# Optimization experiments

Measured on AMD Instinct MI355X. Metric: run time of the kernel, lower is better.

Reference implementation:

```python
import jax, jax.numpy as jnp
import numpy as np

ENC_L, DEC_L = 4, 6
H = 8
D = 512
DFF = 2048
DLAT = 128
NTOK = 1024
NCODES = 2048
NGROUPS = 64
DG = DLAT // NGROUPS  # 2
T_ENC, BT, NSEQ = 128, 8, 16
T_DEC = 1024


def sinusoid_pe(T, d):
    pos = jnp.arange(T, dtype=jnp.float32)[:, None]
    div = jnp.exp(jnp.arange(0, d, 2, dtype=jnp.float32) * (-jnp.log(10000.0) / d))
    pe = jnp.zeros((T, d), jnp.float32)
    pe = pe.at[:, 0::2].set(jnp.sin(pos * div))
    pe = pe.at[:, 1::2].set(jnp.cos(pos * div))
    return pe[:, None, :]  # [T,1,d], seq-first broadcast over batch


def layer_norm(x, g, b):
    m = x.mean(-1, keepdims=True)
    v = ((x - m) ** 2).mean(-1, keepdims=True)
    return (x - m) * jax.lax.rsqrt(v + 1e-5) * g + b


def mha(x, Wqkv, Wo, causal):
    T, B, d = x.shape
    dh = d // H
    q, k, v = jnp.split(x @ Wqkv, 3, axis=-1)
    q = q.reshape(T, B, H, dh)
    k = k.reshape(T, B, H, dh)
    v = v.reshape(T, B, H, dh)
    scores = jnp.einsum('tbhd,sbhd->bhts', q, k) / jnp.sqrt(jnp.float32(dh))
    if causal:
        mask = jnp.tril(jnp.ones((T, T), bool))
        scores = jnp.where(mask[None, None], scores, jnp.float32(-1e9))
    attn = jax.nn.softmax(scores, axis=-1)
    out = jnp.einsum('bhts,sbhd->tbhd', attn, v).reshape(T, B, d)
    return out @ Wo


def tf_layer(x, p, i, causal):
    Wqkv, Wo, ln1g, ln1b, ln2g, ln2b, W1, b1, W2, b2 = [a[i] for a in p]
    x = layer_norm(x + mha(x, Wqkv, Wo, causal), ln1g, ln1b)
    h = jax.nn.relu(x @ W1 + b1) @ W2 + b2
    return layer_norm(x + h, ln2g, ln2b)


def forward_core(enc_inp, dec_inp, dec_inp_seq_pos, fl):
    (emb_table,
     eWqkv, eWo, eln1g, eln1b, eln2g, eln2b, eW1, eb1, eW2, eb2,
     dWqkv, dWo, dln1g, dln1b, dln2g, dln2b, dW1, db1, dW2, db2,
     W_mu, b_mu, codebook, seg_W, seg_b, W_out, b_out) = fl
    scale = jnp.sqrt(jnp.float32(D))
    # token embeddings (seq-first)
    enc_emb = emb_table[enc_inp] * scale            # [T_ENC, BT, NSEQ, D]
    dec_emb = emb_table[dec_inp] * scale            # [T_DEC, BT, D]
    x = enc_emb.reshape(T_ENC, BT * NSEQ, D) + sinusoid_pe(T_ENC, D)
    y = dec_emb + sinusoid_pe(T_DEC, D)
    enc_p = (eWqkv, eWo, eln1g, eln1b, eln2g, eln2b, eW1, eb1, eW2, eb2)
    for i in range(ENC_L):
        x = tf_layer(x, enc_p, i, False)
    mu = x[0] @ W_mu + b_mu                         # [BT*NSEQ, DLAT]
    # grouped vector quantization
    g = mu.reshape(-1, NGROUPS, DG)
    d2 = (g ** 2).sum(-1, keepdims=True) - 2.0 * jnp.einsum('bgd,cd->bgc', g, codebook) + (codebook ** 2).sum(-1)
    idx = jnp.argmin(d2, axis=-1)                   # [BT*NSEQ, NGROUPS]
    q = codebook[idx]
    sg = jax.lax.stop_gradient
    diff = jnp.mean((sg(q) - g) ** 2) + jnp.mean((q - sg(g)) ** 2)
    z = (g + sg(q - g)).reshape(-1, DLAT)           # straight-through
    # ragged scatter of per-segment latents into decoder timeline (vectorized)
    lat = z.reshape(BT, NSEQ, DLAT)
    t = jnp.arange(T_DEC)
    seg = jax.vmap(lambda p: jnp.searchsorted(p, t, side='right') - 1)(dec_inp_seq_pos)  # [BT, T_DEC]
    valid = (seg >= 0) & (seg < NSEQ)
    segc = jnp.clip(seg, 0, NSEQ - 1)
    dec_seg = jnp.where(valid[..., None], lat[jnp.arange(BT)[:, None], segc], 0.0)  # [BT, T_DEC, DLAT]
    dec_seg_emb = dec_seg.transpose(1, 0, 2)        # [T_DEC, BT, DLAT]
    # decoder with in-attention segment conditioning at every layer
    seg_proj = dec_seg_emb @ seg_W + seg_b          # [T_DEC, BT, D]
    dec_p = (dWqkv, dWo, dln1g, dln1b, dln2g, dln2b, dW1, db1, dW2, db2)
    for i in range(DEC_L):
        y = tf_layer(y + seg_proj, dec_p, i, True)
    logits = y @ W_out + b_out                      # [T_DEC, BT, NTOK]
    return mu, z, diff, logits


def setup_inputs() -> dict:
    key = jax.random.key(0)
    ks = jax.random.split(key, 16)
    rn = lambda k, shape, s=0.02: jax.random.normal(k, shape, jnp.float32) * s
    inp = {}
    inp['enc_inp'] = jax.random.randint(ks[0], (T_ENC, BT, NSEQ), 0, NTOK)
    inp['dec_inp'] = jax.random.randint(ks[1], (T_DEC, BT), 0, NTOK)
    inp['dec_inp_seq_pos'] = jnp.sort(jax.random.randint(ks[2], (BT, NSEQ + 1), 0, T_DEC), axis=-1)
    inp['emb_table'] = rn(ks[3], (NTOK, D))
    def stack(kk, L):
        sk = jax.random.split(kk, 4)
        return dict(Wqkv=rn(sk[0], (L, D, 3 * D)), Wo=rn(sk[1], (L, D, D)),
                    ln1g=jnp.ones((L, D)), ln1b=jnp.zeros((L, D)),
                    ln2g=jnp.ones((L, D)), ln2b=jnp.zeros((L, D)),
                    W1=rn(sk[2], (L, D, DFF)), b1=jnp.zeros((L, DFF)),
                    W2=rn(sk[3], (L, DFF, D)), b2=jnp.zeros((L, D)))
    for nm, v in stack(ks[4], ENC_L).items():
        inp['enc_' + nm] = v
    for nm, v in stack(ks[5], DEC_L).items():
        inp['dec_' + nm] = v
    inp['W_mu'] = rn(ks[6], (D, DLAT)); inp['b_mu'] = jnp.zeros((DLAT,))
    inp['codebook'] = rn(ks[7], (NCODES, DG), 1.0)
    inp['seg_W'] = rn(ks[8], (DLAT, D)); inp['seg_b'] = jnp.zeros((D,))
    inp['W_out'] = rn(ks[9], (D, NTOK)); inp['b_out'] = jnp.zeros((NTOK,))
    return inp


def reference(enc_inp, dec_inp, dec_inp_seq_pos, emb_table,
              enc_Wqkv, enc_Wo, enc_ln1g, enc_ln1b, enc_ln2g, enc_ln2b, enc_W1, enc_b1, enc_W2, enc_b2,
              dec_Wqkv, dec_Wo, dec_ln1g, dec_ln1b, dec_ln2g, dec_ln2b, dec_W1, dec_b1, dec_W2, dec_b2,
              W_mu, b_mu, codebook, seg_W, seg_b, W_out, b_out):
    fl = (emb_table,
          enc_Wqkv, enc_Wo, enc_ln1g, enc_ln1b, enc_ln2g, enc_ln2b, enc_W1, enc_b1, enc_W2, enc_b2,
          dec_Wqkv, dec_Wo, dec_ln1g, dec_ln1b, dec_ln2g, dec_ln2b, dec_W1, dec_b1, dec_W2, dec_b2,
          W_mu, b_mu, codebook, seg_W, seg_b, W_out, b_out)
    return forward_core(enc_inp, dec_inp, dec_inp_seq_pos, fl)
```

## Files before the change

### kernel.cpp

```cpp
#include <hip/hip_runtime.h>
#include <hip/hip_bf16.h>


using bf16 = __hip_bfloat16;

#define ENC_L 4
#define DEC_L 6
#define NH    8
#define DMODEL 512
#define DH    64
#define DFF   2048
#define DLAT  128
#define NTOK  1024
#define NCODES 2048
#define T_ENC 128
#define BT    8
#define NSEQ  16
#define T_DEC 1024
#define BENC  (BT*NSEQ)
#define EMB_SCALE 22.627416997969522f
#define LN10000 9.210340371976184f

#define MC 2048
#define ENC_CB 16
// ... 311 lines not shown
        lmax = fmaxf(lmax, dsum);
    }
    red[tid] = lmax; __syncthreads();
    for (int o = 128; o > 0; o >>= 1) {
        if (tid < o) red[tid] = fmaxf(red[tid], red[tid + o]);
        __syncthreads();
    }
    float m = red[0]; __syncthreads();
    float lsum = 0.f;
    for (int s = tid; s < Tlim; s += 256) {
        float e = expf(sc[s] - m);
        sc[s] = e;
        lsum += e;
    }
    red[tid] = lsum; __syncthreads();
    for (int o = 128; o > 0; o >>= 1) {
        if (tid < o) red[tid] += red[tid + o];
        __syncthreads();
    }
    float inv = 1.f / red[0];
    int d = tid & 63, grp = tid >> 6;
    float a = 0.f;
    for (int s = grp; s < Tlim; s += 4)
        a += sc[s] * qkv[((size_t)bl * T + s) * (3 * DMODEL) + 2 * DMODEL + h * DH + d];
    part[tid] = a; __syncthreads();
    if (tid < 64) {
        float o = (part[tid] + part[tid + 64] + part[tid + 128] + part[tid + 192]) * inv;
        out[row * DMODEL + h * DH + tid] = o;
    }
}

__global__ __launch_bounds__(256) void ln_res_kernel(
    const float* __restrict__ a, const float* __restrict__ c,
    const void* __restrict__ g, const void* __restrict__ be, size_t goff,
    float* __restrict__ out, const int* __restrict__ dflag)
{
    int isbf = dflag[0];
    __shared__ float red[256];
    int row = blockIdx.x, tid = threadIdx.x;
    size_t base = (size_t)row * DMODEL;
    float x0 = a[base + tid] + c[base + tid];
    float x1 = a[base + tid + 256] + c[base + tid + 256];
    red[tid] = x0 + x1; __syncthreads();
    for (int o = 128; o > 0; o >>= 1) {
        if (tid < o) red[tid] += red[tid + o];
        __syncthreads();
    }
    float mean = red[0] * (1.f / DMODEL); __syncthreads();
    float d0 = x0 - mean, d1 = x1 - mean;
    red[tid] = d0 * d0 + d1 * d1; __syncthreads();
    for (int o = 128; o > 0; o >>= 1) {
        if (tid < o) red[tid] += red[tid + o];
        __syncthreads();
    }
    float rstd = rsqrtf(red[0] * (1.f / DMODEL) + 1e-5f);
    out[base + tid] = d0 * rstd * ldw(g, goff + tid, isbf) + ldw(be, goff + tid, isbf);
    out[base + tid + 256] = d1 * rstd * ldw(g, goff + tid + 256, isbf) + ldw(be, goff + tid + 256, isbf);
}

__global__ __launch_bounds__(128) void seg_kernel(
    const int* __restrict__ pos, const float* __restrict__ z,
    float* __restrict__ dsc, int b0)
{
    int t = blockIdx.x, bl = blockIdx.y;
    int b = b0 + bl;
    __shared__ int sseg;
    if (threadIdx.x == 0) {
        int cnt = 0;
        for (int i = 0; i < NSEQ + 1; i++) cnt += (pos[b * (NSEQ + 1) + i] <= t) ? 1 : 0;
        sseg = cnt - 1;
    }
    __syncthreads();
    int seg = sseg;
    float v = 0.f;
    if (seg >= 0 && seg < NSEQ) v = z[(b * NSEQ + seg) * DLAT + threadIdx.x];
    dsc[((size_t)bl * T_DEC + t) * DLAT + threadIdx.x] = v;
}


__global__ __launch_bounds__(256) void conv_w_kernel(
    const void* __restrict__ W, unsigned short* __restrict__ WhT,
    unsigned short* __restrict__ WlT, int K, int N, const int* __restrict__ dflag)
{
    int isbf = dflag[0];
    __shared__ float tile[32][33];
    size_t base = (size_t)blockIdx.z * K * N;
    int k0 = blockIdx.y * 32, n0 = blockIdx.x * 32;
    int tx = threadIdx.x & 31, ty = threadIdx.x >> 5;
    #pragma unroll
    for (int i = 0; i < 4; i++)
        tile[ty + 8 * i][tx] = ldw(W, base + (size_t)(k0 + ty + 8 * i) * N + n0 + tx, isbf);
    __syncthreads();
    #pragma unroll
    for (int i = 0; i < 4; i++) {
        float v = tile[tx][ty + 8 * i];
        unsigned short h = f2bf_rne(v);
        size_t o = base + (size_t)(n0 + ty + 8 * i) * K + k0 + tx;
        WhT[o] = h;
        WlT[o] = f2bf_rne(v - bf2f(h));
    }
}

__global__ void conv_vec_kernel(const void* __restrict__ src, float* __restrict__ dst,
                                int n, const int* __restrict__ dflag) {
    int i = blockIdx.x * 256 + threadIdx.x;
    if (i < n) dst[i] = ldw(src, i, dflag[0]);
}

__global__ void embed2_kernel(const int* __restrict__ toks, const void* __restrict__ emb,
                              float* __restrict__ out, unsigned short* __restrict__ oh,
                              unsigned short* __restrict__ ol,
                              int T, int Bdim, int bj0, int total,
                              const int* __restrict__ dflag) {
    int isbf = dflag[0];
    int idx = blockIdx.x * 256 + threadIdx.x;
    if (idx >= total) return;
    int row = idx >> 9;
    int d = idx & 511;
    int bl = row / T;
    int t = row - bl * T;
    int tok = toks[t * Bdim + bj0 + bl];
    float v = ldw(emb, (size_t)tok * DMODEL + d, isbf) * EMB_SCALE;
    int j = d >> 1;
    float freq = expf(-(float)(2 * j) * (LN10000 / (float)DMODEL));
    float ang = (float)t * freq;
    v += (d & 1) ? cosf(ang) : sinf(ang);
    out[idx] = v;
    unsigned short h = f2bf_rne(v);
    oh[idx] = h;
    ol[idx] = f2bf_rne(v - bf2f(h));
}

__global__ void add2_kernel(const float* __restrict__ a, const float* __restrict__ b,
                            float* __restrict__ c, unsigned short* __restrict__ ch,
                            unsigned short* __restrict__ cl, int n) {
    int i = blockIdx.x * 256 + threadIdx.x;
    if (i >= n) return;
    float v = a[i] + b[i];
    c[i] = v;
    unsigned short h = f2bf_rne(v);
    ch[i] = h;
    cl[i] = f2bf_rne(v - bf2f(h));
}

__global__ void gather2_kernel(const float* __restrict__ Xc,
                               unsigned short* __restrict__ agh,
                               unsigned short* __restrict__ agl, int bj0) {
    int bl = blockIdx.x;
    int d = threadIdx.x;
    #pragma unroll
    for (int k = 0; k < 2; k++) {
        int dd = d + k * 256;
        float v = Xc[(size_t)bl * T_ENC * DMODEL + dd];
        size_t o = (size_t)(bj0 + bl) * DMODEL + dd;
        unsigned short h = f2bf_rne(v);
        agh[o] = h;
        agl[o] = f2bf_rne(v - bf2f(h));
    }
}

__global__ __launch_bounds__(128) void seg2_kernel(
    const int* __restrict__ pos, const float* __restrict__ z,
    unsigned short* __restrict__ dh, unsigned short* __restrict__ dl, int b0)
{
    int t = blockIdx.x, bl = blockIdx.y;
    int b = b0 + bl;
    __shared__ int sseg;
    if (threadIdx.x == 0) {
        int cnt = 0;
        for (int i = 0; i < NSEQ + 1; i++) cnt += (pos[b * (NSEQ + 1) + i] <= t) ? 1 : 0;
        sseg = cnt - 1;
    }
    __syncthreads();
    int seg = sseg;
    float v = 0.f;
    if (seg >= 0 && seg < NSEQ) v = z[(b * NSEQ + seg) * DLAT + threadIdx.x];
    size_t o = ((size_t)bl * T_DEC + t) * DLAT + threadIdx.x;
    unsigned short h = f2bf_rne(v);
    dh[o] = h;
    dl[o] = f2bf_rne(v - bf2f(h));
}

__global__ __launch_bounds__(256) void ln_res2_kernel(
    const float* __restrict__ a, const float* __restrict__ c,
    const float* __restrict__ g, const float* __restrict__ be, size_t goff,
    float* __restrict__ out, unsigned short* __restrict__ oh,
    unsigned short* __restrict__ ol)
{
    __shared__ float red[256];
    int row = blockIdx.x, tid = threadIdx.x;
    size_t base = (size_t)row * DMODEL;
    float x0 = a[base + tid] + c[base + tid];
    float x1 = a[base + tid + 256] + c[base + tid + 256];
    red[tid] = x0 + x1; __syncthreads();
    for (int o = 128; o > 0; o >>= 1) {
        if (tid < o) red[tid] += red[tid + o];
        __syncthreads();
    }
    float mean = red[0] * (1.f / DMODEL); __syncthreads();
    float d0 = x0 - mean, d1 = x1 - mean;
    red[tid] = d0 * d0 + d1 * d1; __syncthreads();
    for (int o = 128; o > 0; o >>= 1) {
        if (tid < o) red[tid] += red[tid + o];
        __syncthreads();
    }
    float rstd = rsqrtf(red[0] * (1.f / DMODEL) + 1e-5f);
    float o0 = d0 * rstd * g[goff + tid] + be[goff + tid];
    float o1 = d1 * rstd * g[goff + tid + 256] + be[goff + tid + 256];
    out[base + tid] = o0;
    out[base + tid + 256] = o1;
    unsigned short h0 = f2bf_rne(o0);
    oh[base + tid] = h0;
    ol[base + tid] = f2bf_rne(o0 - bf2f(h0));
    unsigned short h1 = f2bf_rne(o1);
    oh[base + tid + 256] = h1;
    ol[base + tid + 256] = f2bf_rne(o1 - bf2f(h1));
}

__global__ __launch_bounds__(256) void gemm_hl_kernel(
    const unsigned short* __restrict__ Ah, const unsigned short* __restrict__ Al,
    const unsigned short* __restrict__ Wh, const unsigned short* __restrict__ Wl,
    size_t woff, const float* __restrict__ bias, size_t boff,
    float* __restrict__ C, unsigned short* __restrict__ Ch, unsigned short* __restrict__ Cl,
    int M, int N, int K, int relu, int wmode, int b0perm,
    const int* __restrict__ dflag)
{
    int isbf = dflag[0];
    __shared__ unsigned short sAh[4096], sAl[4096], sBh[4096], sBl[4096];
    int tid = threadIdx.x;
    int lane = tid & 63, wave = tid >> 6, quad = lane >> 4, l15 = lane & 15;
    int wm = (wave >> 1) * 32, wn = (wave & 1) * 32;
    int row0 = blockIdx.y * 64, col0 = blockIdx.x * 64;
    int sr = tid >> 3, sc = (tid & 7) * 8;

    floatx4 acc[2][2];
    #pragma unroll
    for (int i = 0; i < 2; i++)
        #pragma unroll
        for (int j = 0; j < 2; j++)
            acc[i][j] = (floatx4){0.f, 0.f, 0.f, 0.f};

    const unsigned short* Wbh = Wh + woff;
    const unsigned short* Wbl = Wl + woff;

    for (int k0 = 0; k0 < K; k0 += 64) {
        #pragma unroll
        for (int rnd = 0; rnd < 2; rnd++) {
            int r = rnd * 32 + sr;
            size_t ga = (size_t)(row0 + r) * K + k0 + sc;
            size_t gb = (size_t)(col0 + r) * K + k0 + sc;
            int di = SWZ(r, sc);
            *(short8*)&sAh[di] = *(const short8*)(const void*)(Ah + ga);
            *(short8*)&sAl[di] = *(const short8*)(const void*)(Al + ga);
            *(short8*)&sBh[di] = *(const short8*)(const void*)(Wbh + gb);
            if (!isbf)
                *(short8*)&sBl[di] = *(const short8*)(const void*)(Wbl + gb);
        }
        __syncthreads();
        if (isbf) {
            #pragma unroll
            for (int ks = 0; ks < 64; ks += 32) {
                short8 fah[2], fal[2], fbh[2];
                #pragma unroll
                for (int i = 0; i < 2; i++) {
                    fah[i] = *(const short8*)&sAh[SWZ(wm + i * 16 + l15, ks + quad * 8)];
                    fal[i] = *(const short8*)&sAl[SWZ(wm + i * 16 + l15, ks + quad * 8)];
                    fbh[i] = *(const short8*)&sBh[SWZ(wn + i * 16 + l15, ks + quad * 8)];
                }
                #pragma unroll
                for (int i = 0; i < 2; i++)
                    #pragma unroll
                    for (int j = 0; j < 2; j++) {
                        acc[i][j] = __builtin_amdgcn_mfma_f32_16x16x32_bf16(fah[i], fbh[j], acc[i][j], 0, 0, 0);
                        acc[i][j] = __builtin_amdgcn_mfma_f32_16x16x32_bf16(fal[i], fbh[j], acc[i][j], 0, 0, 0);
                    }
            }
        } else {
            #pragma unroll
            for (int ks = 0; ks < 64; ks += 32) {
                short8 fah[2], fal[2], fbh[2], fbl[2];
                #pragma unroll
                for (int i = 0; i < 2; i++) {
                    fah[i] = *(const short8*)&sAh[SWZ(wm + i * 16 + l15, ks + quad * 8)];
                    fal[i] = *(const short8*)&sAl[SWZ(wm + i * 16 + l15, ks + quad * 8)];
                    fbh[i] = *(const short8*)&sBh[SWZ(wn + i * 16 + l15, ks + quad * 8)];
                    fbl[i] = *(const short8*)&sBl[SWZ(wn + i * 16 + l15, ks + quad * 8)];
                }
                #pragma unroll
                for (int i = 0; i < 2; i++)
                    #pragma unroll
                    for (int j = 0; j < 2; j++) {
                        acc[i][j] = __builtin_amdgcn_mfma_f32_16x16x32_bf16(fah[i], fbh[j], acc[i][j], 0, 0, 0);
                        acc[i][j] = __builtin_amdgcn_mfma_f32_16x16x32_bf16(fal[i], fbh[j], acc[i][j], 0, 0, 0);
                        acc[i][j] = __builtin_amdgcn_mfma_f32_16x16x32_bf16(fah[i], fbl[j], acc[i][j], 0, 0, 0);
                    }
            }
        }
        __syncthreads();
    }
    #pragma unroll
    for (int i = 0; i < 2; i++) {
        #pragma unroll
        for (int j = 0; j < 2; j++) {
            int gc = col0 + wn + j * 16 + l15;
            float bv = bias ? bias[boff + gc] : 0.f;
            #pragma unroll
            for (int r = 0; r < 4; r++) {
                int gr = row0 + wm + i * 16 + quad * 4 + r;
                float v = acc[i][j][r] + bv;
                if (relu) v = fmaxf(v, 0.f);
                size_t orow = (size_t)gr;
                if (b0perm >= 0) orow = (size_t)((gr & (T_DEC - 1)) * BT + b0perm + (gr >> 10));
                if (wmode & 1) C[orow * N + gc] = v;
                if (wmode & 2) {
                    unsigned short hh = f2bf_rne(v);
                    Ch[(size_t)gr * N + gc] = hh;
                    Cl[(size_t)gr * N + gc] = f2bf_rne(v - bf2f(hh));
                }
            }
        }
    }
}

__global__ __launch_bounds__(256) void v_prep_kernel(
    const unsigned short* __restrict__ QKVh, const unsigned short* __restrict__ QKVl,
    unsigned short* __restrict__ VhT, unsigned short* __restrict__ VlT, int T)
{
    __shared__ unsigned short th[64][72], tl[64][72];
    int tid = threadIdx.x;
    int r0 = blockIdx.x * 64;
    int vc0 = blockIdx.y * 64;
    int sr = tid >> 3, sc = (tid & 7) * 8;
    #pragma unroll
    for (int rnd = 0; rnd < 2; rnd++) {
        int rr = rnd * 32 + sr;
        size_t o = (size_t)(r0 + rr) * 1536 + 1024 + vc0 + sc;
        *(short8*)&th[rr][sc] = *(const short8*)(const void*)(QKVh + o);
        *(short8*)&tl[rr][sc] = *(const short8*)(const void*)(QKVl + o);
    }
    __syncthreads();
    int bl = r0 / T;
    int t0 = r0 - bl * T;
    #pragma unroll
    for (int rnd = 0; rnd < 2; rnd++) {
        int dr = rnd * 32 + sr;
        int gd = vc0 + dr;
        int hh = gd >> 6, dd = gd & 63;
        size_t obase = ((size_t)(bl * NH + hh) * 64 + dd) * T + t0 + sc;
        short8 hv, lv;
        #pragma unroll
        for (int i = 0; i < 8; i++) {
            hv[i] = (short)th[sc + i][dr];
            lv[i] = (short)tl[sc + i][dr];
        }
        *(short8*)&VhT[obase] = hv;
        *(short8*)&VlT[obase] = lv;
    }
}

__global__ __launch_bounds__(256) void attn_flash_kernel(
    const unsigned short* __restrict__ QKVh, const unsigned short* __restrict__ QKVl,
    const unsigned short* __restrict__ VhT, const unsigned short* __restrict__ VlT,
    unsigned short* __restrict__ AOh, unsigned short* __restrict__ AOl,
    int T, int causal)
{
    __shared__ unsigned short sQh[4096], sQl[4096], sKh[4096], sKl[4096],
                              sVh[4096], sVl[4096], sPh[4096], sPl[4096];
    int tid = threadIdx.x;
    int lane = tid & 63, wave = tid >> 6, quad = lane >> 4, l15 = lane & 15;
    int q0 = blockIdx.x * 64;
    int bl = blockIdx.y >> 3, h = blockIdx.y & 7;
    int sr = tid >> 3, sc = (tid & 7) * 8;
    int wq = wave * 16;
    size_t rowbase = (size_t)bl * T;
    size_t vbase = (size_t)(bl * NH + h) * 64;

    #pragma unroll
    for (int rnd = 0; rnd < 2; rnd++) {
        int r = rnd * 32 + sr;
        size_t o = (rowbase + q0 + r) * 1536 + h * 64 + sc;
        int di = SWZ(r, sc);
        *(short8*)&sQh[di] = *(const short8*)(const void*)(QKVh + o);
        *(short8*)&sQl[di] = *(const short8*)(const void*)(QKVl + o);
    }

    floatx4 acco[4];
    #pragma unroll
    for (int jd = 0; jd < 4; jd++) acco[jd] = (floatx4){0.f, 0.f, 0.f, 0.f};
    float m_old[4], lsum[4];
    #pragma unroll
    for (int r = 0; r < 4; r++) { m_old[r] = -1e30f; lsum[r] = 0.f; }

    int smax = causal ? q0 : (T - 64);
    for (int s0 = 0; s0 <= smax; s0 += 64) {
        #pragma unroll
        for (int rnd = 0; rnd < 2; rnd++) {
            int r = rnd * 32 + sr;
            int di = SWZ(r, sc);
            size_t ko = (rowbase + s0 + r) * 1536 + 512 + h * 64 + sc;
            *(short8*)&sKh[di] = *(const short8*)(const void*)(QKVh + ko);
            *(short8*)&sKl[di] = *(const short8*)(const void*)(QKVl + ko);
            size_t vo = (vbase + r) * T + s0 + sc;
            *(short8*)&sVh[di] = *(const short8*)(const void*)(VhT + vo);
            *(short8*)&sVl[di] = *(const short8*)(const void*)(VlT + vo);
        }
        __syncthreads();

        floatx4 accs[4];
        #pragma unroll
        for (int j = 0; j < 4; j++) accs[j] = (floatx4){0.f, 0.f, 0.f, 0.f};
        #pragma unroll
        for (int ks = 0; ks < 64; ks += 32) {
            short8 qh = *(const short8*)&sQh[SWZ(wq + l15, ks + quad * 8)];
            short8 ql = *(const short8*)&sQl[SWZ(wq + l15, ks + quad * 8)];
            #pragma unroll
            for (int j = 0; j < 4; j++) {
                short8 kh = *(const short8*)&sKh[SWZ(j * 16 + l15, ks + quad * 8)];
                short8 kl = *(const short8*)&sKl[SWZ(j * 16 + l15, ks + quad * 8)];
                accs[j] = __builtin_amdgcn_mfma_f32_16x16x32_bf16(qh, kh, accs[j], 0, 0, 0);
                accs[j] = __builtin_amdgcn_mfma_f32_16x16x32_bf16(ql, kh, accs[j], 0, 0, 0);
                accs[j] = __builtin_amdgcn_mfma_f32_16x16x32_bf16(qh, kl, accs[j], 0, 0, 0);
            }
        }

        float f[4];
        #pragma unroll
        for (int r = 0; r < 4; r++) {
            int qg = q0 + wq + quad * 4 + r;
            float tm = -1e30f;
            #pragma unroll
            for (int j = 0; j < 4; j++) {
                float s = accs[j][r] * 0.125f;
                if (causal && (s0 + j * 16 + l15 > qg)) s = -1e30f;
                accs[j][r] = s;
                tm = fmaxf(tm, s);
            }
            #pragma unroll
            for (int mk = 1; mk < 16; mk <<= 1)
                tm = fmaxf(tm, __shfl_xor(tm, mk, 64));
            float mn = fmaxf(m_old[r], tm);
            float fr = __expf(m_old[r] - mn);
            float ts = 0.f;
            #pragma unroll
            for (int j = 0; j < 4; j++) {
                float p = __expf(accs[j][r] - mn);
                accs[j][r] = p;
                ts += p;
            }
            #pragma unroll
            for (int mk = 1; mk < 16; mk <<= 1)
                ts += __shfl_xor(ts, mk, 64);
            lsum[r] = lsum[r] * fr + ts;
            m_old[r] = mn;
            f[r] = fr;
        }
        #pragma unroll
        for (int jd = 0; jd < 4; jd++)
            #pragma unroll
            for (int r = 0; r < 4; r++)
                acco[jd][r] *= f[r];

        #pragma unroll
        for (int j = 0; j < 4; j++)
            #pragma unroll
            for (int r = 0; r < 4; r++) {
                float p = accs[j][r];
                unsigned short ph = f2bf_rne(p);
                int idx = SWZ(wq + quad * 4 + r, j * 16 + l15);
                sPh[idx] = ph;
                sPl[idx] = f2bf_rne(p - bf2f(ph));
            }
        __syncthreads();

        #pragma unroll
        for (int ks = 0; ks < 64; ks += 32) {
            short8 ph = *(const short8*)&sPh[SWZ(wq + l15, ks + quad * 8)];
            short8 pl = *(const short8*)&sPl[SWZ(wq + l15, ks + quad * 8)];
            #pragma unroll
            for (int jd = 0; jd < 4; jd++) {
                short8 vh = *(const short8*)&sVh[SWZ(jd * 16 + l15, ks + quad * 8)];
                short8 vl = *(const short8*)&sVl[SWZ(jd * 16 + l15, ks + quad * 8)];
                acco[jd] = __builtin_amdgcn_mfma_f32_16x16x32_bf16(ph, vh, acco[jd], 0, 0, 0);
                acco[jd] = __builtin_amdgcn_mfma_f32_16x16x32_bf16(pl, vh, acco[jd], 0, 0, 0);
                acco[jd] = __builtin_amdgcn_mfma_f32_16x16x32_bf16(ph, vl, acco[jd], 0, 0, 0);
            }
        }
        __syncthreads();
    }

    #pragma unroll
    for (int jd = 0; jd < 4; jd++) {
        #pragma unroll
        for (int r = 0; r < 4; r++) {
            int qr = q0 + wq + quad * 4 + r;
            float o = acco[jd][r] / lsum[r];
            size_t oo = (rowbase + qr) * 512 + h * 64 + jd * 16 + l15;
            unsigned short hh = f2bf_rne(o);
            AOh[oo] = hh;
            AOl[oo] = f2bf_rne(o - bf2f(hh));
        }
    }
}


static const size_t OFF_EWQKV = 0;
static const size_t OFF_EWO   = OFF_EWQKV + (size_t)4 * 512 * 1536;
static const size_t OFF_EW1   = OFF_EWO   + (size_t)4 * 512 * 512;
static const size_t OFF_EW2   = OFF_EW1   + (size_t)4 * 512 * 2048;
static const size_t OFF_DWQKV = OFF_EW2   + (size_t)4 * 2048 * 512;
static const size_t OFF_DWO   = OFF_DWQKV + (size_t)6 * 512 * 1536;
static const size_t OFF_DW1   = OFF_DWO   + (size_t)6 * 512 * 512;
static const size_t OFF_DW2   = OFF_DW1   + (size_t)6 * 512 * 2048;
static const size_t OFF_WMU   = OFF_DW2   + (size_t)6 * 2048 * 512;
static const size_t OFF_SEGW  = OFF_WMU   + (size_t)512 * 128;
static const size_t OFF_WOUT  = OFF_SEGW  + (size_t)128 * 512;
static const size_t W_TOTAL   = OFF_WOUT  + (size_t)512 * 1024;

static const size_t VELN1G = 0;
static const size_t VELN1B = VELN1G + 2048;
static const size_t VELN2G = VELN1B + 2048;
static const size_t VELN2B = VELN2G + 2048;
static const size_t VDLN1G = VELN2B + 2048;
static const size_t VDLN1B = VDLN1G + 3072;
static const size_t VDLN2G = VDLN1B + 3072;
static const size_t VDLN2B = VDLN2G + 3072;
static const size_t VEB1   = VDLN2B + 3072;
static const size_t VEB2   = VEB1 + 8192;
static const size_t VDB1   = VEB2 + 2048;
static const size_t VDB2   = VDB1 + 12288;
static const size_t VBMU   = VDB2 + 3072;
static const size_t VSEGB  = VBMU + 128;
static const size_t VBOUT  = VSEGB + 512;
static const size_t VEC_TOTAL = VBOUT + 1024;

extern "C" void kernel_launch(void* const* d_in, const int* in_sizes, int n_in,
                              void* d_out, int out_size, void* d_ws, size_t ws_size,
                              hipStream_t stream)
{
    const int*  enc_inp = (const int*)d_in[0];
    const int*  dec_inp = (const int*)d_in[1];
    const int*  seq_pos = (const int*)d_in[2];
    const void* emb   = d_in[3];
    const void* eWqkv = d_in[4];  const void* eWo  = d_in[5];
    const void* eln1g = d_in[6];  const void* eln1b = d_in[7];
    const void* eln2g = d_in[8];  const void* eln2b = d_in[9];
    const void* eW1   = d_in[10]; const void* eb1  = d_in[11];
    const void* eW2   = d_in[12]; const void* eb2  = d_in[13];
    const void* dWqkv = d_in[14]; const void* dWo  = d_in[15];
    const void* dln1g = d_in[16]; const void* dln1b = d_in[17];
    const void* dln2g = d_in[18]; const void* dln2b = d_in[19];
    const void* dW1   = d_in[20]; const void* db1  = d_in[21];
    const void* dW2   = d_in[22]; const void* db2  = d_in[23];
    const void* W_mu  = d_in[24]; const void* b_mu = d_in[25];
    const void* cbk   = d_in[26];
    const void* seg_W = d_in[27]; const void* seg_b = d_in[28];
    const void* W_out = d_in[29]; const void* b_out = d_in[30];

    float* outf = (float*)d_out;
    float* out_mu     = outf;
    float* out_z      = outf + 16384;
    float* out_diff   = outf + 32768;
    float* out_logits = outf + 32769;

    bool order_ok = (n_in == 31) &&
        in_sizes[0] == 16384 && in_sizes[1] == 8192 && in_sizes[2] == 136 &&
        in_sizes[3] == 524288 && in_sizes[4] == 3145728 && in_sizes[5] == 1048576 &&
        in_sizes[10] == 4194304 && in_sizes[14] == 4718592 && in_sizes[15] == 1572864 &&
        in_sizes[24] == 65536 && in_sizes[25] == 128 && in_sizes[26] == 4096 &&
        in_sizes[29] == 524288 && in_sizes[30] == 1024;
    if (!order_ok) {
        fill_kernel<<<64, 256, 0, stream>>>(out_mu, 100.0f, 16384);
        return;
    }

    float *XC = nullptr, *SPC = nullptr, *TIN = nullptr, *Pb = nullptr,
          *MU = nullptr, *Z = nullptr, *ACC = nullptr, *VECS = nullptr;
    unsigned short *XCh = nullptr, *XCl = nullptr, *TINh = nullptr, *TINl = nullptr,
                   *QKVh = nullptr, *QKVl = nullptr, *VhT = nullptr, *VlT = nullptr,
                   *AOh = nullptr, *AOl = nullptr, *Hh = nullptr, *Hl = nullptr,
                   *DSCh = nullptr, *DSCl = nullptr, *AGh = nullptr, *AGl = nullptr,
                   *WH = nullptr, *WL = nullptr;
    int* FLG = nullptr;

    auto layout = [&](size_t R) -> size_t {
        char* p = (char*)d_ws;
        auto al = [&](size_t b) -> char* {
            char* q = p; p += (b + 255) & ~(size_t)255; return q;
        };
        size_t Rd = R;
        XC   = (float*)al(R * 512 * 4);
        XCh  = (unsigned short*)al(R * 512 * 2);
        XCl  = (unsigned short*)al(R * 512 * 2);
        SPC  = (float*)al(Rd * 512 * 4);
        TIN  = (float*)al(Rd * 512 * 4);
        TINh = (unsigned short*)al(Rd * 512 * 2);
        TINl = (unsigned short*)al(Rd * 512 * 2);
        QKVh = (unsigned short*)al(R * 1536 * 2);
        QKVl = (unsigned short*)al(R * 1536 * 2);
        VhT  = (unsigned short*)al(R * 512 * 2);
        VlT  = (unsigned short*)al(R * 512 * 2);
        AOh  = (unsigned short*)al(R * 512 * 2);
        AOl  = (unsigned short*)al(R * 512 * 2);
        Pb   = (float*)al(R * 512 * 4);
        Hh   = (unsigned short*)al(R * 2048 * 2);
        Hl   = (unsigned short*)al(R * 2048 * 2);
        DSCh = (unsigned short*)al(Rd * 128 * 2);
        DSCl = (unsigned short*)al(Rd * 128 * 2);
        AGh  = (unsigned short*)al((size_t)128 * 512 * 2);
        AGl  = (unsigned short*)al((size_t)128 * 512 * 2);
        MU   = (float*)al((size_t)128 * 128 * 4);
        Z    = (float*)al((size_t)128 * 128 * 4);
        ACC  = (float*)al(256);
        FLG  = (int*)al(256);
        VECS = (float*)al(VEC_TOTAL * 4);
        WH   = (unsigned short*)al(W_TOTAL * 2);
        WL   = (unsigned short*)al(W_TOTAL * 2);
        return (size_t)(p - (char*)d_ws);
    };

    size_t R = 0;
    {
        const size_t cands[3] = {8192, 4096, 2048};
        for (int ci = 0; ci < 3; ci++) {
            if (layout(cands[ci]) <= ws_size) { R = cands[ci]; break; }
        }
    }

    if (R) {
        layout(R);
        int enc_cb = (int)(R / 128); if (enc_cb > 128) enc_cb = 128;
        int dec_cb = (int)(R / 1024); if (dec_cb > 8) dec_cb = 8;
        int rows_e = enc_cb * T_ENC;
        int rows_d = dec_cb * T_DEC;

        detect_kernel<<<1, 64, 0, stream>>>((const unsigned int*)eln1g, FLG, ACC);

        conv_w_kernel<<<dim3(1536/32, 512/32, 4), 256, 0, stream>>>(eWqkv, WH+OFF_EWQKV, WL+OFF_EWQKV, 512, 1536, FLG);
        conv_w_kernel<<<dim3( 512/32, 512/32, 4), 256, 0, stream>>>(eWo,   WH+OFF_EWO,   WL+OFF_EWO,   512,  512, FLG);
        conv_w_kernel<<<dim3(2048/32, 512/32, 4), 256, 0, stream>>>(eW1,   WH+OFF_EW1,   WL+OFF_EW1,   512, 2048, FLG);
        conv_w_kernel<<<dim3( 512/32,2048/32, 4), 256, 0, stream>>>(eW2,   WH+OFF_EW2,   WL+OFF_EW2,  2048,  512, FLG);
        conv_w_kernel<<<dim3(1536/32, 512/32, 6), 256, 0, stream>>>(dWqkv, WH+OFF_DWQKV, WL+OFF_DWQKV, 512, 1536, FLG);
        conv_w_kernel<<<dim3( 512/32, 512/32, 6), 256, 0, stream>>>(dWo,   WH+OFF_DWO,   WL+OFF_DWO,   512,  512, FLG);
        conv_w_kernel<<<dim3(2048/32, 512/32, 6), 256, 0, stream>>>(dW1,   WH+OFF_DW1,   WL+OFF_DW1,   512, 2048, FLG);
        conv_w_kernel<<<dim3( 512/32,2048/32, 6), 256, 0, stream>>>(dW2,   WH+OFF_DW2,   WL+OFF_DW2,  2048,  512, FLG);
        conv_w_kernel<<<dim3( 128/32, 512/32, 1), 256, 0, stream>>>(W_mu,  WH+OFF_WMU,   WL+OFF_WMU,   512,  128, FLG);
        conv_w_kernel<<<dim3( 512/32, 128/32, 1), 256, 0, stream>>>(seg_W, WH+OFF_SEGW,  WL+OFF_SEGW,  128,  512, FLG);
        conv_w_kernel<<<dim3(1024/32, 512/32, 1), 256, 0, stream>>>(W_out, WH+OFF_WOUT,  WL+OFF_WOUT,  512, 1024, FLG);

        conv_vec_kernel<<<8, 256, 0, stream>>>(eln1g, VECS+VELN1G, 2048, FLG);
        conv_vec_kernel<<<8, 256, 0, stream>>>(eln1b, VECS+VELN1B, 2048, FLG);
        conv_vec_kernel<<<8, 256, 0, stream>>>(eln2g, VECS+VELN2G, 2048, FLG);
        conv_vec_kernel<<<8, 256, 0, stream>>>(eln2b, VECS+VELN2B, 2048, FLG);
        conv_vec_kernel<<<12, 256, 0, stream>>>(dln1g, VECS+VDLN1G, 3072, FLG);
        conv_vec_kernel<<<12, 256, 0, stream>>>(dln1b, VECS+VDLN1B, 3072, FLG);
        conv_vec_kernel<<<12, 256, 0, stream>>>(dln2g, VECS+VDLN2G, 3072, FLG);
        conv_vec_kernel<<<12, 256, 0, stream>>>(dln2b, VECS+VDLN2B, 3072, FLG);
        conv_vec_kernel<<<32, 256, 0, stream>>>(eb1, VECS+VEB1, 8192, FLG);
        conv_vec_kernel<<<8, 256, 0, stream>>>(eb2, VECS+VEB2, 2048, FLG);
        conv_vec_kernel<<<48, 256, 0, stream>>>(db1, VECS+VDB1, 12288, FLG);
        conv_vec_kernel<<<12, 256, 0, stream>>>(db2, VECS+VDB2, 3072, FLG);
        conv_vec_kernel<<<1, 256, 0, stream>>>(b_mu, VECS+VBMU, 128, FLG);
        conv_vec_kernel<<<2, 256, 0, stream>>>(seg_b, VECS+VSEGB, 512, FLG);
        conv_vec_kernel<<<4, 256, 0, stream>>>(b_out, VECS+VBOUT, 1024, FLG);

        for (int c = 0; c < BENC / enc_cb; c++) {
            int bj0 = c * enc_cb;
            int tot = rows_e * DMODEL;
            embed2_kernel<<<(tot + 255) / 256, 256, 0, stream>>>(
                enc_inp, emb, XC, XCh, XCl, T_ENC, BENC, bj0, tot, FLG);
            for (int i = 0; i < ENC_L; i++) {
                size_t oQ = (size_t)i * 512 * 1536, oO = (size_t)i * 512 * 512;
                size_t o1 = (size_t)i * 512 * 2048, o2 = (size_t)i * 2048 * 512;
                gemm_hl_kernel<<<dim3(24, rows_e / 64), 256, 0, stream>>>(
                    XCh, XCl, WH+OFF_EWQKV, WL+OFF_EWQKV, oQ, nullptr, 0,
                    nullptr, QKVh, QKVl, rows_e, 1536, 512, 0, 2, -1, FLG);
                v_prep_kernel<<<dim3(rows_e / 64, 8), 256, 0, stream>>>(
                    QKVh, QKVl, VhT, VlT, T_ENC);
                attn_flash_kernel<<<dim3(T_ENC / 64, enc_cb * NH), 256, 0, stream>>>(
                    QKVh, QKVl, VhT, VlT, AOh, AOl, T_ENC, 0);
                gemm_hl_kernel<<<dim3(8, rows_e / 64), 256, 0, stream>>>(
                    AOh, AOl, WH+OFF_EWO, WL+OFF_EWO, oO, nullptr, 0,
                    Pb, nullptr, nullptr, rows_e, 512, 512, 0, 1, -1, FLG);
                ln_res2_kernel<<<rows_e, 256, 0, stream>>>(XC, Pb, VECS+VELN1G, VECS+VELN1B,
                    (size_t)i*512, XC, XCh, XCl);
                gemm_hl_kernel<<<dim3(32, rows_e / 64), 256, 0, stream>>>(
                    XCh, XCl, WH+OFF_EW1, WL+OFF_EW1, o1, VECS+VEB1, (size_t)i*2048,
                    nullptr, Hh, Hl, rows_e, 2048, 512, 1, 2, -1, FLG);
                gemm_hl_kernel<<<dim3(8, rows_e / 64), 256, 0, stream>>>(
                    Hh, Hl, WH+OFF_EW2, WL+OFF_EW2, o2, VECS+VEB2, (size_t)i*512,
                    Pb, nullptr, nullptr, rows_e, 512, 2048, 0, 1, -1, FLG);
                ln_res2_kernel<<<rows_e, 256, 0, stream>>>(XC, Pb, VECS+VELN2G, VECS+VELN2B,
                    (size_t)i*512, XC, XCh, XCl);
            }
            gather2_kernel<<<enc_cb, 256, 0, stream>>>(XC, AGh, AGl, bj0);
        }

        gemm_hl_kernel<<<dim3(2, 2), 256, 0, stream>>>(
            AGh, AGl, WH+OFF_WMU, WL+OFF_WMU, 0, VECS+VBMU, 0,
            MU, nullptr, nullptr, BENC, 128, 512, 0, 1, -1, FLG);
        vq_kernel<<<BENC, 64, 0, stream>>>(MU, cbk, Z, ACC, FLG);
        copy_kernel<<<64, 256, 0, stream>>>(MU, out_mu, 16384);
        copy_kernel<<<64, 256, 0, stream>>>(Z, out_z, 16384);
        diff_kernel<<<1, 1, 0, stream>>>(ACC, out_diff);

        for (int c = 0; c < BT / dec_cb; c++) {
            int b0 = c * dec_cb;
            seg2_kernel<<<dim3(T_DEC, dec_cb), 128, 0, stream>>>(seq_pos, Z, DSCh, DSCl, b0);
            gemm_hl_kernel<<<dim3(8, rows_d / 64), 256, 0, stream>>>(
                DSCh, DSCl, WH+OFF_SEGW, WL+OFF_SEGW, 0, VECS+VSEGB, 0,
                SPC, nullptr, nullptr, rows_d, 512, 128, 0, 1, -1, FLG);
            int tot = rows_d * DMODEL;
            embed2_kernel<<<(tot + 255) / 256, 256, 0, stream>>>(
                dec_inp, emb, XC, XCh, XCl, T_DEC, BT, b0, tot, FLG);
            for (int i = 0; i < DEC_L; i++) {
                size_t oQ = (size_t)i * 512 * 1536, oO = (size_t)i * 512 * 512;
                size_t o1 = (size_t)i * 512 * 2048, o2 = (size_t)i * 2048 * 512;
                add2_kernel<<<(tot + 255) / 256, 256, 0, stream>>>(
                    XC, SPC, TIN, TINh, TINl, tot);
                gemm_hl_kernel<<<dim3(24, rows_d / 64), 256, 0, stream>>>(
                    TINh, TINl, WH+OFF_DWQKV, WL+OFF_DWQKV, oQ, nullptr, 0,
                    nullptr, QKVh, QKVl, rows_d, 1536, 512, 0, 2, -1, FLG);
                v_prep_kernel<<<dim3(rows_d / 64, 8), 256, 0, stream>>>(
                    QKVh, QKVl, VhT, VlT, T_DEC);
                attn_flash_kernel<<<dim3(T_DEC / 64, dec_cb * NH), 256, 0, stream>>>(
                    QKVh, QKVl, VhT, VlT, AOh, AOl, T_DEC, 1);
                gemm_hl_kernel<<<dim3(8, rows_d / 64), 256, 0, stream>>>(
                    AOh, AOl, WH+OFF_DWO, WL+OFF_DWO, oO, nullptr, 0,
                    Pb, nullptr, nullptr, rows_d, 512, 512, 0, 1, -1, FLG);
                ln_res2_kernel<<<rows_d, 256, 0, stream>>>(TIN, Pb, VECS+VDLN1G, VECS+VDLN1B,
                    (size_t)i*512, TIN, TINh, TINl);
                gemm_hl_kernel<<<dim3(32, rows_d / 64), 256, 0, stream>>>(
                    TINh, TINl, WH+OFF_DW1, WL+OFF_DW1, o1, VECS+VDB1, (size_t)i*2048,
                    nullptr, Hh, Hl, rows_d, 2048, 512, 1, 2, -1, FLG);
                gemm_hl_kernel<<<dim3(8, rows_d / 64), 256, 0, stream>>>(
                    Hh, Hl, WH+OFF_DW2, WL+OFF_DW2, o2, VECS+VDB2, (size_t)i*512,
                    Pb, nullptr, nullptr, rows_d, 512, 2048, 0, 1, -1, FLG);
                ln_res2_kernel<<<rows_d, 256, 0, stream>>>(TIN, Pb, VECS+VDLN2G, VECS+VDLN2B,
                    (size_t)i*512, XC, XCh, XCl);
            }
            gemm_hl_kernel<<<dim3(16, rows_d / 64), 256, 0, stream>>>(
                XCh, XCl, WH+OFF_WOUT, WL+OFF_WOUT, 0, VECS+VBOUT, 0,
                out_logits, nullptr, nullptr, rows_d, 1024, 512, 0, 1, b0, FLG);
        }
        return;
    }

    float* ws  = (float*)d_ws;
    float* oXC  = ws;
    float* oSPC = ws + 1048576;
    float* oTIN = ws + 2097152;
    float* oQKV = ws + 3145728;
    float* oAO  = ws + 6291456;
    float* oH   = ws + 3145728;
    float* oP   = ws + 7340032;
    float* oDSC = ws + 8388608;
    float* oAG  = ws + 8650752;
    float* oMU  = ws + 8716288;
    float* oZ   = ws + 8732672;
    float* oACC = ws + 8749056;
    int*   oFLG = (int*)(ws + 8749057);

    detect_kernel<<<1, 64, 0, stream>>>((const unsigned int*)eln1g, oFLG, oACC);

    for (int c = 0; c < BENC / ENC_CB; c++) {
        int bj0 = c * ENC_CB;
        embed_kernel<<<(MC * DMODEL + 255) / 256, 256, 0, stream>>>(
            enc_inp, emb, oXC, T_ENC, BENC, bj0, ENC_CB, oFLG);
        for (int i = 0; i < ENC_L; i++) {
            size_t oQ  = (size_t)i * DMODEL * 3 * DMODEL;
            size_t oO  = (size_t)i * DMODEL * DMODEL;
            size_t o1  = (size_t)i * DMODEL * DFF;
            size_t o2  = (size_t)i * DFF * DMODEL;
            size_t oLn = (size_t)i * DMODEL;
            size_t oB1 = (size_t)i * DFF;
            gemm_mfma_kernel<<<dim3(3 * DMODEL / 64, MC / 64), 256, 0, stream>>>(
                oXC, eWqkv, oQ, nullptr, 0, oQKV, MC, 3 * DMODEL, DMODEL, 0, oFLG);
            attn_kernel<<<dim3(T_ENC, ENC_CB * NH), 256, 0, stream>>>(oQKV, oAO, T_ENC, 0);
            gemm_mfma_kernel<<<dim3(DMODEL / 64, MC / 64), 256, 0, stream>>>(
                oAO, eWo, oO, nullptr, 0, oP, MC, DMODEL, DMODEL, 0, oFLG);
            ln_res_kernel<<<MC, 256, 0, stream>>>(oXC, oP, eln1g, eln1b, oLn, oXC, oFLG);
            gemm_mfma_kernel<<<dim3(DFF / 64, MC / 64), 256, 0, stream>>>(
                oXC, eW1, o1, eb1, oB1, oH, MC, DFF, DMODEL, 1, oFLG);
            gemm_mfma_kernel<<<dim3(DMODEL / 64, MC / 64), 256, 0, stream>>>(
                oH, eW2, o2, eb2, oLn, oP, MC, DMODEL, DFF, 0, oFLG);
            ln_res_kernel<<<MC, 256, 0, stream>>>(oXC, oP, eln2g, eln2b, oLn, oXC, oFLG);
        }
        gather_t0_kernel<<<ENC_CB, 256, 0, stream>>>(oXC, oAG, bj0);
    }

    gemm_mfma_kernel<<<dim3(DLAT / 64, BENC / 64), 256, 0, stream>>>(
        oAG, W_mu, 0, b_mu, 0, oMU, BENC, DLAT, DMODEL, 0, oFLG);
    vq_kernel<<<BENC, 64, 0, stream>>>(oMU, cbk, oZ, oACC, oFLG);
    copy_kernel<<<64, 256, 0, stream>>>(oMU, out_mu, 16384);
    copy_kernel<<<64, 256, 0, stream>>>(oZ, out_z, 16384);
    diff_kernel<<<1, 1, 0, stream>>>(oACC, out_diff);

    for (int c = 0; c < BT / DEC_CB; c++) {
        int b0 = c * DEC_CB;
        seg_kernel<<<dim3(T_DEC, DEC_CB), 128, 0, stream>>>(seq_pos, oZ, oDSC, b0);
        gemm_mfma_kernel<<<dim3(DMODEL / 64, MC / 64), 256, 0, stream>>>(
            oDSC, seg_W, 0, seg_b, 0, oSPC, MC, DMODEL, DLAT, 0, oFLG);
        embed_kernel<<<(MC * DMODEL + 255) / 256, 256, 0, stream>>>(
            dec_inp, emb, oXC, T_DEC, BT, b0, DEC_CB, oFLG);
        for (int i = 0; i < DEC_L; i++) {
            size_t oQ  = (size_t)i * DMODEL * 3 * DMODEL;
            size_t oO  = (size_t)i * DMODEL * DMODEL;
            size_t o1  = (size_t)i * DMODEL * DFF;
            size_t o2  = (size_t)i * DFF * DMODEL;
            size_t oLn = (size_t)i * DMODEL;
            size_t oB1 = (size_t)i * DFF;
            add_kernel<<<(MC * DMODEL + 255) / 256, 256, 0, stream>>>(oXC, oSPC, oTIN, MC * DMODEL);
            gemm_mfma_kernel<<<dim3(3 * DMODEL / 64, MC / 64), 256, 0, stream>>>(
                oTIN, dWqkv, oQ, nullptr, 0, oQKV, MC, 3 * DMODEL, DMODEL, 0, oFLG);
            attn_kernel<<<dim3(T_DEC, DEC_CB * NH), 256, 0, stream>>>(oQKV, oAO, T_DEC, 1);
            gemm_mfma_kernel<<<dim3(DMODEL / 64, MC / 64), 256, 0, stream>>>(
                oAO, dWo, oO, nullptr, 0, oP, MC, DMODEL, DMODEL, 0, oFLG);
            ln_res_kernel<<<MC, 256, 0, stream>>>(oTIN, oP, dln1g, dln1b, oLn, oTIN, oFLG);
            gemm_mfma_kernel<<<dim3(DFF / 64, MC / 64), 256, 0, stream>>>(
                oTIN, dW1, o1, db1, oB1, oH, MC, DFF, DMODEL, 1, oFLG);
            gemm_mfma_kernel<<<dim3(DMODEL / 64, MC / 64), 256, 0, stream>>>(
                oH, dW2, o2, db2, oLn, oP, MC, DMODEL, DFF, 0, oFLG);
            ln_res_kernel<<<MC, 256, 0, stream>>>(oTIN, oP, dln2g, dln2b, oLn, oXC, oFLG);
        }
        gemm_mfma_logits_kernel<<<dim3(NTOK / 64, MC / 64), 256, 0, stream>>>(
            oXC, W_out, b_out, out_logits, NTOK, DMODEL, b0, oFLG);
    }
}
```

Before: 6.826 ms.

## Add 128x128-tile split-bf16 GEMM kernel for wide-N projections

Adds a new GEMM kernel with a 128x128 output tile per block (each wave computing 64x64) and uses it for the QKV, FFN1 and output-logit projections. The larger tile increases data reuse from shared memory and MFMA work per load, and the low-half weight tile is loaded in a second pass only when the weights are not plain bf16. The cost is more accumulator registers and fewer blocks per launch, which may lower occupancy on the smaller encoder GEMMs.

```diff
diff --git a/kernel.cpp b/kernel.cpp
--- a/kernel.cpp
+++ b/kernel.cpp
@@ -637,6 +637,113 @@
     for (int i = 0; i < 2; i++) {
         #pragma unroll
         for (int j = 0; j < 2; j++) {
+            int gc = col0 + wn + j * 16 + l15;
+            float bv = bias ? bias[boff + gc] : 0.f;
+            #pragma unroll
+            for (int r = 0; r < 4; r++) {
+                int gr = row0 + wm + i * 16 + quad * 4 + r;
+                float v = acc[i][j][r] + bv;
+                if (relu) v = fmaxf(v, 0.f);
+                size_t orow = (size_t)gr;
+                if (b0perm >= 0) orow = (size_t)((gr & (T_DEC - 1)) * BT + b0perm + (gr >> 10));
+                if (wmode & 1) C[orow * N + gc] = v;
+                if (wmode & 2) {
+                    unsigned short hh = f2bf_rne(v);
+                    Ch[(size_t)gr * N + gc] = hh;
+                    Cl[(size_t)gr * N + gc] = f2bf_rne(v - bf2f(hh));
+                }
+            }
+        }
+    }
+}
+
+__global__ __launch_bounds__(256) void gemm128_kernel(
+    const unsigned short* __restrict__ Ah, const unsigned short* __restrict__ Al,
+    const unsigned short* __restrict__ Wh, const unsigned short* __restrict__ Wl,
+    size_t woff, const float* __restrict__ bias, size_t boff,
+    float* __restrict__ C, unsigned short* __restrict__ Ch, unsigned short* __restrict__ Cl,
+    int M, int N, int K, int relu, int wmode, int b0perm,
+    const int* __restrict__ dflag)
+{
+    int isbf = dflag[0];
+    __shared__ unsigned short sAh[8192], sAl[8192], sBx[8192];
+    int tid = threadIdx.x;
+    int lane = tid & 63, wave = tid >> 6, quad = lane >> 4, l15 = lane & 15;
+    int wm = (wave >> 1) * 64, wn = (wave & 1) * 64;
+    int row0 = blockIdx.y * 128, col0 = blockIdx.x * 128;
+    int sr = tid >> 3, sc = (tid & 7) * 8;
+
+    floatx4 acc[4][4];
+    #pragma unroll
+    for (int i = 0; i < 4; i++)
+        #pragma unroll
+        for (int j = 0; j < 4; j++)
+            acc[i][j] = (floatx4){0.f, 0.f, 0.f, 0.f};
+
+    const unsigned short* Wbh = Wh + woff;
+    const unsigned short* Wbl = Wl + woff;
+
+    for (int k0 = 0; k0 < K; k0 += 64) {
+        #pragma unroll
+        for (int rnd = 0; rnd < 4; rnd++) {
+            int r = rnd * 32 + sr;
+            size_t ga = (size_t)(row0 + r) * K + k0 + sc;
+            size_t gb = (size_t)(col0 + r) * K + k0 + sc;
+            int di = SWZ(r, sc);
+            *(short8*)&sAh[di] = *(const short8*)(const void*)(Ah + ga);
+            *(short8*)&sAl[di] = *(const short8*)(const void*)(Al + ga);
+            *(short8*)&sBx[di] = *(const short8*)(const void*)(Wbh + gb);
+        }
+        __syncthreads();
+        #pragma unroll
+        for (int ks = 0; ks < 64; ks += 32) {
+            short8 fah[4], fal[4];
+            #pragma unroll
+            for (int i = 0; i < 4; i++) {
+                fah[i] = *(const short8*)&sAh[SWZ(wm + i * 16 + l15, ks + quad * 8)];
+                fal[i] = *(const short8*)&sAl[SWZ(wm + i * 16 + l15, ks + quad * 8)];
+            }
+            #pragma unroll
+            for (int j = 0; j < 4; j++) {
+                short8 fbh = *(const short8*)&sBx[SWZ(wn + j * 16 + l15, ks + quad * 8)];
+                #pragma unroll
+                for (int i = 0; i < 4; i++) {
+                    acc[i][j] = __builtin_amdgcn_mfma_f32_16x16x32_bf16(fah[i], fbh, acc[i][j], 0, 0, 0);
+                    acc[i][j] = __builtin_amdgcn_mfma_f32_16x16x32_bf16(fal[i], fbh, acc[i][j], 0, 0, 0);
+                }
+            }
+        }
+        __syncthreads();
+        if (!isbf) {
+            #pragma unroll
+            for (int rnd = 0; rnd < 4; rnd++) {
+                int r = rnd * 32 + sr;
+                size_t gb = (size_t)(col0 + r) * K + k0 + sc;
+                int di = SWZ(r, sc);
+                *(short8*)&sBx[di] = *(const short8*)(const void*)(Wbl + gb);
+            }
+            __syncthreads();
+            #pragma unroll
+            for (int ks = 0; ks < 64; ks += 32) {
+                short8 fah[4];
+                #pragma unroll
+                for (int i = 0; i < 4; i++)
+                    fah[i] = *(const short8*)&sAh[SWZ(wm + i * 16 + l15, ks + quad * 8)];
+                #pragma unroll
+                for (int j = 0; j < 4; j++) {
+                    short8 fbl = *(const short8*)&sBx[SWZ(wn + j * 16 + l15, ks + quad * 8)];
+                    #pragma unroll
+                    for (int i = 0; i < 4; i++)
+                        acc[i][j] = __builtin_amdgcn_mfma_f32_16x16x32_bf16(fah[i], fbl, acc[i][j], 0, 0, 0);
+                }
+            }
+            __syncthreads();
+        }
+    }
+    #pragma unroll
+    for (int i = 0; i < 4; i++) {
+        #pragma unroll
+        for (int j = 0; j < 4; j++) {
             int gc = col0 + wn + j * 16 + l15;
             float bv = bias ? bias[boff + gc] : 0.f;
             #pragma unroll
@@ -1006,7 +1113,7 @@
             for (int i = 0; i < ENC_L; i++) {
                 size_t oQ = (size_t)i * 512 * 1536, oO = (size_t)i * 512 * 512;
                 size_t o1 = (size_t)i * 512 * 2048, o2 = (size_t)i * 2048 * 512;
-                gemm_hl_kernel<<<dim3(24, rows_e / 64), 256, 0, stream>>>(
+                gemm128_kernel<<<dim3(12, rows_e / 128), 256, 0, stream>>>(
                     XCh, XCl, WH+OFF_EWQKV, WL+OFF_EWQKV, oQ, nullptr, 0,
                     nullptr, QKVh, QKVl, rows_e, 1536, 512, 0, 2, -1, FLG);
                 v_prep_kernel<<<dim3(rows_e / 64, 8), 256, 0, stream>>>(
@@ -1018,7 +1125,7 @@
                     Pb, nullptr, nullptr, rows_e, 512, 512, 0, 1, -1, FLG);
                 ln_res2_kernel<<<rows_e, 256, 0, stream>>>(XC, Pb, VECS+VELN1G, VECS+VELN1B,
                     (size_t)i*512, XC, XCh, XCl);
-                gemm_hl_kernel<<<dim3(32, rows_e / 64), 256, 0, stream>>>(
+                gemm128_kernel<<<dim3(16, rows_e / 128), 256, 0, stream>>>(
                     XCh, XCl, WH+OFF_EW1, WL+OFF_EW1, o1, VECS+VEB1, (size_t)i*2048,
                     nullptr, Hh, Hl, rows_e, 2048, 512, 1, 2, -1, FLG);
                 gemm_hl_kernel<<<dim3(8, rows_e / 64), 256, 0, stream>>>(
@@ -1052,7 +1159,7 @@
                 size_t o1 = (size_t)i * 512 * 2048, o2 = (size_t)i * 2048 * 512;
                 add2_kernel<<<(tot + 255) / 256, 256, 0, stream>>>(
                     XC, SPC, TIN, TINh, TINl, tot);
-                gemm_hl_kernel<<<dim3(24, rows_d / 64), 256, 0, stream>>>(
+                gemm128_kernel<<<dim3(12, rows_d / 128), 256, 0, stream>>>(
                     TINh, TINl, WH+OFF_DWQKV, WL+OFF_DWQKV, oQ, nullptr, 0,
                     nullptr, QKVh, QKVl, rows_d, 1536, 512, 0, 2, -1, FLG);
                 v_prep_kernel<<<dim3(rows_d / 64, 8), 256, 0, stream>>>(
@@ -1064,7 +1171,7 @@
                     Pb, nullptr, nullptr, rows_d, 512, 512, 0, 1, -1, FLG);
                 ln_res2_kernel<<<rows_d, 256, 0, stream>>>(TIN, Pb, VECS+VDLN1G, VECS+VDLN1B,
                     (size_t)i*512, TIN, TINh, TINl);
-                gemm_hl_kernel<<<dim3(32, rows_d / 64), 256, 0, stream>>>(
+                gemm128_kernel<<<dim3(16, rows_d / 128), 256, 0, stream>>>(
                     TINh, TINl, WH+OFF_DW1, WL+OFF_DW1, o1, VECS+VDB1, (size_t)i*2048,
                     nullptr, Hh, Hl, rows_d, 2048, 512, 1, 2, -1, FLG);
                 gemm_hl_kernel<<<dim3(8, rows_d / 64), 256, 0, stream>>>(
@@ -1073,7 +1180,7 @@
                 ln_res2_kernel<<<rows_d, 256, 0, stream>>>(TIN, Pb, VECS+VDLN2G, VECS+VDLN2B,
                     (size_t)i*512, XC, XCh, XCl);
             }
-            gemm_hl_kernel<<<dim3(16, rows_d / 64), 256, 0, stream>>>(
+            gemm128_kernel<<<dim3(8, rows_d / 128), 256, 0, stream>>>(
                 XCh, XCl, WH+OFF_WOUT, WL+OFF_WOUT, 0, VECS+VBOUT, 0,
                 out_logits, nullptr, nullptr, rows_d, 1024, 512, 0, 1, b0, FLG);
         }
```

Result: no change. 6.696 ms (-1.9%).
